# Kernel optimization log

Measured on AMD Instinct MI355X. Metric: run time of the kernel, lower is better.

Reference implementation:

```python
import jax, jax.numpy as jnp
import numpy as np

B_POINTS = 1024   # batch of independent spatial points
NF = 672          # hourly forcing samples (28 days * 24 h)

def setup_inputs() -> dict:
    key = jax.random.key(0)
    k1, k2, k3 = jax.random.split(key, 3)
    # pk ~ [-10, -9] as in the source, with small perturbation
    pk = jnp.array([-10.0, -9.0], jnp.float32) + 0.1 * jax.random.normal(k1, (2,), jnp.float32)
    # wind stress ~ O(0.1) N/m^2
    TAx = 0.1 * jax.random.normal(k2, (B_POINTS, NF), jnp.float32)
    TAy = 0.1 * jax.random.normal(k3, (B_POINTS, NF), jnp.float32)
    fc = jnp.float32(1e-4)  # Coriolis frequency
    return {"pk": pk, "TAx": TAx, "TAy": TAy, "fc": fc,
            "nt": 40320, "dt": 60, "dt_forcing": 3600}

def reference(pk, TAx, TAy, fc, nt, dt, dt_forcing):
    # Slab-ocean 1D model, explicit Euler (difx=True branch of the source):
    #   dU/dt =  fc*V + K0*TAx(t) - K1*U
    #   dV/dt = -fc*U + K0*TAy(t) - K1*V
    # with TAx/TAy linearly interpolated from hourly forcing to the dt grid.
    K = jnp.exp(pk)                       # [2]
    nsub = dt_forcing // dt               # substeps per forcing sample (60)
    nf = TAx.shape[-1]                    # number of forcing samples
    dtf = jnp.float32(dt)

    def step(carry, it):
        U, V = carry                      # [B], [B]
        itf = it // nsub
        aa = (jnp.mod(it, nsub) / nsub).astype(jnp.float32)
        itsup = jnp.where(itf + 1 >= nf, nf - 1, itf + 1)
        tax = (1.0 - aa) * TAx[:, itf] + aa * TAx[:, itsup]
        tay = (1.0 - aa) * TAy[:, itf] + aa * TAy[:, itsup]
        Un = U + dtf * ( fc * V + K[0] * tax - K[1] * U)
        Vn = V + dtf * (-fc * U + K[0] * tay - K[1] * V)
        return (Un, Vn), Un

    B = TAx.shape[0]
    U0 = jnp.zeros((B,), jnp.float32)
    _, Us = jax.lax.scan(step, (U0, U0), jnp.arange(nt, dtype=jnp.int32))
    return Us  # [nt, B] zonal velocity saved after each Euler step
```

## Files before the change

### kernel.cpp

```cpp
#include <hip/hip_runtime.h>


#define NT    40320
#define BPTS  1024
#define NF    672
#define NSUB  60
#define CH    60
#define NCH   (NT / CH)
#define CG    2
#define NPAIR (NCH / CG)
#define PPT   4
#define NW    32
#define NV    (NW / 4)
#define TP    256
#define NTILE (BPTS / TP)
#define NXCD  8

typedef float vf4 __attribute__((ext_vector_type(4)));

__device__ __forceinline__ void gload_lds16(const float* g, float* l) {
    __builtin_amdgcn_global_load_lds(
        (const __attribute__((address_space(1))) void*)g,
        (__attribute__((address_space(3))) void*)l, 16, 0, 0);
}

__global__ __launch_bounds__(256, 2)
void slab_chunk(const float* __restrict__ pk,
                const float* __restrict__ TAx,
                const float* __restrict__ TAy,
                const float* __restrict__ fcp,
                const int* __restrict__ dtp,
                float* __restrict__ out) {
    const int bid = blockIdx.x;
    const int kp  = (bid & (NXCD - 1)) * (NPAIR / NXCD) + (bid >> 3);
    const int k0  = kp * CG;
    const int tid = threadIdx.x;

    const float dtf = (float)dtp[0];
    const float K0  = expf(pk[0]);
    const float K1  = expf(pk[1]);
    const float ar  = 1.0f - dtf * K1;
    const float ai  = -dtf * fcp[0];
    const float bs  = dtf * K0;

    float g1r = 0.f, g1i = 0.f, g2r = 0.f, g2i = 0.f;
    float pr = 1.f, pi = 0.f;
    for (int m = 0; m < NSUB; ++m) {
        g1r += pr; g1i += pi;
        float w = (float)(NSUB - 1 - m) * (1.0f / NSUB);
        g2r = fmaf(w, pr, g2r); g2i = fmaf(w, pi, g2i);
        float nr = pr * ar - pi * ai;
        float ni = pr * ai + pi * ar;
        pr = nr; pi = ni;
    }
    const float Ar  = pr,        Ai  = pi;
    const float cAr = g1r - g2r, cAi = g1i - g2i;
    const float cBr = g2r,       cBi = g2i;
    const float cCr = cAr + (Ar * cBr - Ai * cBi);
    const float cCi = cAi + (Ar * cBi + Ai * cBr);

    int va = (k0 + 4) & ~3;
    if (va > NF) va = NF;
    const int ja = va - NW;

    float wgtR[NW], wgtI[NW];
    {
        float Wr = 1.f, Wi = 0.f;
#pragma unroll
        for (int i = NW - 1; i >= 0; --i) {
            const int m = ja + i;
            float er = 0.f, ei = 0.f;
            if (k0 > 0 && m >= 0 && m <= k0) {
                if (m == k0) { er = cBr; ei = cBi; }
                else {
                    const float br = (m == 0) ? cAr : cCr;
                    const float bi = (m == 0) ? cAi : cCi;
                    er = Wr * br - Wi * bi;
                    ei = Wr * bi + Wi * br;
                    const float t2 = Wr * Ar - Wi * Ai;
                    Wi = Wr * Ai + Wi * Ar; Wr = t2;
                }
            }
            wgtR[i] = er; wgtI[i] = ei;
        }
    }

    __shared__ float ldsx[TP][NW];
    __shared__ float ldsy[TP][NW];
    float zr4[NTILE], zi4[NTILE];

#pragma unroll
    for (int tau = 0; tau < NTILE; ++tau) {
#pragma unroll
        for (int it = 0; it < NV; ++it) {
            const int V  = tid + 256 * it;
            const int r  = V >> 3;
            const int u  = V & 7;
            const int uu = u ^ (r & 7);
            int off = ja + 4 * uu; if (off < 0) off = 0;
            const size_t gb = (size_t)(tau * TP + r) * NF + off;
            gload_lds16(TAx + gb, &ldsx[0][0] + (size_t)V * 4);
            gload_lds16(TAy + gb, &ldsy[0][0] + (size_t)V * 4);
        }
        __syncthreads();

        float aR = 0.f, aI = 0.f;
#pragma unroll
        for (int v = 0; v < NV; ++v) {
            const int sv = v ^ (tid & 7);
            const vf4 fx = *(const vf4*)&ldsx[tid][4 * sv];
            const vf4 fy = *(const vf4*)&ldsy[tid][4 * sv];
#pragma unroll
            for (int e = 0; e < 4; ++e) {
                const int i = 4 * v + e;
                aR = fmaf(wgtR[i], fx[e], fmaf(-wgtI[i], fy[e], aR));
                aI = fmaf(wgtR[i], fy[e], fmaf( wgtI[i], fx[e], aI));
            }
        }
        zr4[tau] = bs * aR; zi4[tau] = bs * aI;
        __syncthreads();
    }

    float2* zbuf = (float2*)&ldsx[0][0];
#pragma unroll
    for (int tau = 0; tau < NTILE; ++tau)
        zbuf[tau * TP + tid] = make_float2(zr4[tau], zi4[tau]);
    __syncthreads();

    const int p0 = tid * PPT;
    float zr[PPT], zi[PPT];
#pragma unroll
    for (int j = 0; j < PPT; ++j) {
        float2 z = zbuf[p0 + j];
        zr[j] = z.x; zi[j] = z.y;
    }

    float x0[PPT], y0[PPT];
#pragma unroll
    for (int j = 0; j < PPT; ++j) {
        x0[j] = TAx[(size_t)(p0 + j) * NF + k0];
        y0[j] = TAy[(size_t)(p0 + j) * NF + k0];
    }

    float* orow = out + (size_t)k0 * CH * BPTS + p0;

    for (int c = 0; c < CG; ++c) {
        const int kk = k0 + c;
        const int f1 = (kk + 1 < NF) ? kk + 1 : NF - 1;

        float x1[PPT], y1[PPT], bx[PPT], by[PPT], dbx[PPT], dby[PPT];
#pragma unroll
        for (int j = 0; j < PPT; ++j) {
            x1[j] = TAx[(size_t)(p0 + j) * NF + f1];
            y1[j] = TAy[(size_t)(p0 + j) * NF + f1];
            bx[j]  = bs * x0[j];
            by[j]  = bs * y0[j];
            dbx[j] = bs * (x1[j] - x0[j]) * (1.0f / NSUB);
            dby[j] = bs * (y1[j] - y0[j]) * (1.0f / NSUB);
        }

#pragma unroll 10
        for (int s = 0; s < CH; ++s) {
#pragma unroll
            for (int j = 0; j < PPT; ++j) {
                const float ur = fmaf(ar, zr[j], fmaf(-ai, zi[j], bx[j]));
                const float vi = fmaf(ar, zi[j], fmaf( ai, zr[j], by[j]));
                zr[j] = ur; zi[j] = vi;
                bx[j] += dbx[j]; by[j] += dby[j];
            }
            vf4 v; v.x = zr[0]; v.y = zr[1]; v.z = zr[2]; v.w = zr[3];
            __builtin_nontemporal_store(v, (vf4*)orow);
            orow += BPTS;
        }

#pragma unroll
        for (int j = 0; j < PPT; ++j) { x0[j] = x1[j]; y0[j] = y1[j]; }
    }
}

extern "C" void kernel_launch(void* const* d_in, const int* in_sizes, int n_in,
                              void* d_out, int out_size, void* d_ws, size_t ws_size,
                              hipStream_t stream) {
    const float* pk  = (const float*)d_in[0];
    const float* TAx = (const float*)d_in[1];
    const float* TAy = (const float*)d_in[2];
    const float* fcp = (const float*)d_in[3];
    const int*   dtp = (const int*)d_in[5];
    float* out = (float*)d_out;

    slab_chunk<<<NPAIR, 256, 0, stream>>>(pk, TAx, TAy, fcp, dtp, out);
}
```

Before: 49.01 us.

## Split time axis into 80-step blocks straddling forcing chunks

Each block now covers 80 consecutive output rows instead of two whole 60-step chunks, giving 504 blocks instead of 336, which should balance better across CUs and XCDs. A block starts at an arbitrary substep inside a forcing chunk, so it first advances the state through the skipped substeps without storing, then writes the rest of that chunk and part of the next one. The catch-up steps add redundant recurrence work, and every block still repeats the full 32-tap window prologue, so total prologue and LDS load work grows with the larger block count.

```diff
diff --git a/kernel.cpp b/kernel.cpp
--- a/kernel.cpp
+++ b/kernel.cpp
@@ -7,14 +7,15 @@
 #define NSUB  60
 #define CH    60
 #define NCH   (NT / CH)
-#define CG    2
-#define NPAIR (NCH / CG)
+#define RPB   80
+#define NBLK  (NT / RPB)
 #define PPT   4
 #define NW    32
 #define NV    (NW / 4)
 #define TP    256
 #define NTILE (BPTS / TP)
 #define NXCD  8
+#define BPX   (NBLK / NXCD)
 
 typedef float vf4 __attribute__((ext_vector_type(4)));
 
@@ -32,8 +33,10 @@
                 const int* __restrict__ dtp,
                 float* __restrict__ out) {
     const int bid = blockIdx.x;
-    const int kp  = (bid & (NXCD - 1)) * (NPAIR / NXCD) + (bid >> 3);
-    const int k0  = kp * CG;
+    const int swz = (bid & (NXCD - 1)) * BPX + (bid >> 3);
+    const int g0  = swz * RPB;
+    const int k0  = g0 / CH;
+    const int s0  = g0 - k0 * CH;
     const int tid = threadIdx.x;
 
     const float dtf = (float)dtp[0];
@@ -135,46 +138,74 @@
         zr[j] = z.x; zi[j] = z.y;
     }
 
-    float x0[PPT], y0[PPT];
+    const int f1a = (k0 + 1 < NF) ? k0 + 1 : NF - 1;
+    float x1[PPT], y1[PPT], bx[PPT], by[PPT], dbx[PPT], dby[PPT];
 #pragma unroll
     for (int j = 0; j < PPT; ++j) {
-        x0[j] = TAx[(size_t)(p0 + j) * NF + k0];
-        y0[j] = TAy[(size_t)(p0 + j) * NF + k0];
-    }
-
-    float* orow = out + (size_t)k0 * CH * BPTS + p0;
-
-    for (int c = 0; c < CG; ++c) {
-        const int kk = k0 + c;
-        const int f1 = (kk + 1 < NF) ? kk + 1 : NF - 1;
-
-        float x1[PPT], y1[PPT], bx[PPT], by[PPT], dbx[PPT], dby[PPT];
+        const float* rx = TAx + (size_t)(p0 + j) * NF;
+        const float* ry = TAy + (size_t)(p0 + j) * NF;
+        const float x0 = rx[k0], y0 = ry[k0];
+        x1[j] = rx[f1a]; y1[j] = ry[f1a];
+        bx[j]  = bs * x0;
+        by[j]  = bs * y0;
+        dbx[j] = bs * (x1[j] - x0) * (1.0f / NSUB);
+        dby[j] = bs * (y1[j] - y0) * (1.0f / NSUB);
+    }
+
+    for (int s = 0; s < s0; ++s) {
 #pragma unroll
         for (int j = 0; j < PPT; ++j) {
-            x1[j] = TAx[(size_t)(p0 + j) * NF + f1];
-            y1[j] = TAy[(size_t)(p0 + j) * NF + f1];
-            bx[j]  = bs * x0[j];
-            by[j]  = bs * y0[j];
-            dbx[j] = bs * (x1[j] - x0[j]) * (1.0f / NSUB);
-            dby[j] = bs * (y1[j] - y0[j]) * (1.0f / NSUB);
-        }
-
+            const float ur = fmaf(ar, zr[j], fmaf(-ai, zi[j], bx[j]));
+            const float vi = fmaf(ar, zi[j], fmaf( ai, zr[j], by[j]));
+            zr[j] = ur; zi[j] = vi;
+            bx[j] += dbx[j]; by[j] += dby[j];
+        }
+    }
+
+    float* orow = out + (size_t)g0 * BPTS + p0;
+
+    const int n1 = CH - s0;
 #pragma unroll 10
-        for (int s = 0; s < CH; ++s) {
-#pragma unroll
-            for (int j = 0; j < PPT; ++j) {
-                const float ur = fmaf(ar, zr[j], fmaf(-ai, zi[j], bx[j]));
-                const float vi = fmaf(ar, zi[j], fmaf( ai, zr[j], by[j]));
-                zr[j] = ur; zi[j] = vi;
-                bx[j] += dbx[j]; by[j] += dby[j];
-            }
-            vf4 v; v.x = zr[0]; v.y = zr[1]; v.z = zr[2]; v.w = zr[3];
-            __builtin_nontemporal_store(v, (vf4*)orow);
-            orow += BPTS;
-        }
-
-#pragma unroll
-        for (int j = 0; j < PPT; ++j) { x0[j] = x1[j]; y0[j] = y1[j]; }
+    for (int s = 0; s < n1; ++s) {
+#pragma unroll
+        for (int j = 0; j < PPT; ++j) {
+            const float ur = fmaf(ar, zr[j], fmaf(-ai, zi[j], bx[j]));
+            const float vi = fmaf(ar, zi[j], fmaf( ai, zr[j], by[j]));
+            zr[j] = ur; zi[j] = vi;
+            bx[j] += dbx[j]; by[j] += dby[j];
+        }
+        vf4 v; v.x = zr[0]; v.y = zr[1]; v.z = zr[2]; v.w = zr[3];
+        __builtin_nontemporal_store(v, (vf4*)orow);
+        orow += BPTS;
+    }
+
+    const int k1  = k0 + 1;
+    const int f1b = (k1 + 1 < NF) ? k1 + 1 : NF - 1;
+#pragma unroll
+    for (int j = 0; j < PPT; ++j) {
+        const float* rx = TAx + (size_t)(p0 + j) * NF;
+        const float* ry = TAy + (size_t)(p0 + j) * NF;
+        const float x0 = x1[j], y0 = y1[j];
+        const float xn = rx[f1b], yn = ry[f1b];
+        bx[j]  = bs * x0;
+        by[j]  = bs * y0;
+        dbx[j] = bs * (xn - x0) * (1.0f / NSUB);
+        dby[j] = bs * (yn - y0) * (1.0f / NSUB);
+    }
+
+    const int n2 = RPB - n1;
+#pragma unroll 10
+    for (int s = 0; s < n2; ++s) {
+#pragma unroll
+        for (int j = 0; j < PPT; ++j) {
+            const float ur = fmaf(ar, zr[j], fmaf(-ai, zi[j], bx[j]));
+            const float vi = fmaf(ar, zi[j], fmaf( ai, zr[j], by[j]));
+            zr[j] = ur; zi[j] = vi;
+            bx[j] += dbx[j]; by[j] += dby[j];
+        }
+        vf4 v; v.x = zr[0]; v.y = zr[1]; v.z = zr[2]; v.w = zr[3];
+        __builtin_nontemporal_store(v, (vf4*)orow);
+        orow += BPTS;
     }
 }
 
@@ -188,5 +219,5 @@
     const int*   dtp = (const int*)d_in[5];
     float* out = (float*)d_out;
 
-    slab_chunk<<<NPAIR, 256, 0, stream>>>(pk, TAx, TAy, fcp, dtp, out);
+    slab_chunk<<<NBLK, 256, 0, stream>>>(pk, TAx, TAy, fcp, dtp, out);
 }
```

Result: no change. 49.59 us (+1.2%).
